# Kernel optimization log

Hardware: AMD Instinct MI355X
Metric: run time of the kernel (lower is better)

## Reference

```python
import jax, jax.numpy as jnp
import numpy as np

E, C, H, I = 8, 4096, 1024, 4096

def setup_inputs() -> dict:
    key = jax.random.key(0)
    k_x, k_g, k_u, k_d = jax.random.split(key, 4)
    scale_h = 1.0 / np.sqrt(H)
    scale_i = 1.0 / np.sqrt(I)
    return {
        "x_routed": jax.random.normal(k_x, (E, C, H), dtype=jnp.float32),
        "W_gate": jax.random.normal(k_g, (E, H, I), dtype=jnp.float32) * scale_h,
        "W_up": jax.random.normal(k_u, (E, H, I), dtype=jnp.float32) * scale_h,
        "W_down": jax.random.normal(k_d, (E, I, H), dtype=jnp.float32) * scale_i,
    }

def reference(x_routed, W_gate, W_up, W_down):
    # Per-expert SwiGLU MLP, batched over the expert axis as a grouped GEMM.
    # gate = silu(x @ Wg); up = x @ Wu; out = (gate * up) @ Wd
    gate = jax.nn.silu(jnp.einsum("ech,ehi->eci", x_routed, W_gate))
    up = jnp.einsum("ech,ehi->eci", x_routed, W_up)
    out = jnp.einsum("eci,eih->ech", gate * up, W_down)
    return out
```

## Files before the change

kernel.cpp:

```cpp
#include <hip/hip_runtime.h>
#include <hip/hip_bf16.h>
#include <stdint.h>
#include <stddef.h>

#define E_ 8
#define C_ 4096
#define H_ 1024
#define I_ 4096

typedef short s16;
typedef __attribute__((ext_vector_type(8))) short short8;
typedef __attribute__((ext_vector_type(4))) short short4v;
typedef __attribute__((ext_vector_type(4))) float f32x4;
typedef __attribute__((ext_vector_type(4))) float float4v;

__device__ __forceinline__ s16 f2bf(float f) {
  union { __hip_bfloat16 h; s16 s; } u;
  u.h = __float2bfloat16(f);
  return u.s;
}

__device__ __forceinline__ void gload16(const void* gsrc, void* ldst) {
  __builtin_amdgcn_global_load_lds(
      (const __attribute__((address_space(1))) void*)gsrc,
      (__attribute__((address_space(3))) void*)ldst, 16, 0, 0);
}

__global__ __launch_bounds__(256) void prep_kernel(
    const float* __restrict__ x, const float* __restrict__ Wg,
    const float* __restrict__ Wu, const float* __restrict__ Wd,
    s16* __restrict__ xb, s16* __restrict__ Wgu, s16* __restrict__ WdT)
{
  __shared__ float tile[64][65];
  const int t = threadIdx.x;
  const int z = blockIdx.z;
  const size_t e = blockIdx.y;

  if (z == 0) {
    size_t base = e * (size_t)C_ * H_ + ((size_t)blockIdx.x * 256 + t) * 16;
    for (int j = 0; j < 16; j += 8) {
      float4v v0 = *(const float4v*)(x + base + j);
      float4v v1 = *(const float4v*)(x + base + j + 4);
      s16 o[8];
      o[0] = f2bf(v0[0]); o[1] = f2bf(v0[1]); o[2] = f2bf(v0[2]); o[3] = f2bf(v0[3]);
      o[4] = f2bf(v1[0]); o[5] = f2bf(v1[1]); o[6] = f2bf(v1[2]); o[7] = f2bf(v1[3]);
      *(short8*)(xb + base + j) = *(short8*)o;
    }
    return;
  }

  const float* src; int Cc;
  if (z == 1)      { src = Wg + e * (size_t)H_ * I_; Cc = I_; }
  else if (z == 2) { src = Wu + e * (size_t)H_ * I_; Cc = I_; }
  else             { src = Wd + e * (size_t)H_ * I_; Cc = H_; }

  const int tpr  = Cc >> 6;
  const int trow = blockIdx.x / tpr;
  const int tcol = blockIdx.x % tpr;

  const int c = t & 63, rq = t >> 6;
  for (int i = 0; i < 16; ++i) {
    int r = rq * 16 + i;
    tile[r][c] = src[(size_t)(trow * 64 + r) * Cc + tcol * 64 + c];
  }
  __syncthreads();

  const int ro = t >> 2, cb = (t & 3) * 16;
  s16 o[16];
  for (int j = 0; j < 16; ++j) o[j] = f2bf(tile[cb + j][ro]);

  const int i0 = tcol * 64 + ro;
  s16* op;
  if (z == 3) {
    op = WdT + e * (size_t)H_ * I_ + (size_t)i0 * I_ + trow * 64 + cb;
  } else {
    int grow = ((i0 & ~15) << 1) + (i0 & 15) + ((z == 2) ? 16 : 0);
    op = Wgu + e * (size_t)2 * I_ * H_ + (size_t)grow * H_ + trow * 64 + cb;
  }
  *(short8*)op       = *(short8*)&o[0];
  *(short8*)(op + 8) = *(short8*)&o[8];
}

#define MFMA16(MH, A0, A1, A2, A3)                                                            \
  acc[(MH)*4+0][0] = __builtin_amdgcn_mfma_f32_16x16x32_bf16(bf[0], A0, acc[(MH)*4+0][0],0,0,0); \
  acc[(MH)*4+0][1] = __builtin_amdgcn_mfma_f32_16x16x32_bf16(bf[1], A0, acc[(MH)*4+0][1],0,0,0); \
  acc[(MH)*4+0][2] = __builtin_amdgcn_mfma_f32_16x16x32_bf16(bf[2], A0, acc[(MH)*4+0][2],0,0,0); \
  acc[(MH)*4+0][3] = __builtin_amdgcn_mfma_f32_16x16x32_bf16(bf[3], A0, acc[(MH)*4+0][3],0,0,0); \
  acc[(MH)*4+1][0] = __builtin_amdgcn_mfma_f32_16x16x32_bf16(bf[0], A1, acc[(MH)*4+1][0],0,0,0); \
  acc[(MH)*4+1][1] = __builtin_amdgcn_mfma_f32_16x16x32_bf16(bf[1], A1, acc[(MH)*4+1][1],0,0,0); \
  acc[(MH)*4+1][2] = __builtin_amdgcn_mfma_f32_16x16x32_bf16(bf[2], A1, acc[(MH)*4+1][2],0,0,0); \
  acc[(MH)*4+1][3] = __builtin_amdgcn_mfma_f32_16x16x32_bf16(bf[3], A1, acc[(MH)*4+1][3],0,0,0); \
  acc[(MH)*4+2][0] = __builtin_amdgcn_mfma_f32_16x16x32_bf16(bf[0], A2, acc[(MH)*4+2][0],0,0,0); \
  acc[(MH)*4+2][1] = __builtin_amdgcn_mfma_f32_16x16x32_bf16(bf[1], A2, acc[(MH)*4+2][1],0,0,0); \
  acc[(MH)*4+2][2] = __builtin_amdgcn_mfma_f32_16x16x32_bf16(bf[2], A2, acc[(MH)*4+2][2],0,0,0); \
  acc[(MH)*4+2][3] = __builtin_amdgcn_mfma_f32_16x16x32_bf16(bf[3], A2, acc[(MH)*4+2][3],0,0,0); \
  acc[(MH)*4+3][0] = __builtin_amdgcn_mfma_f32_16x16x32_bf16(bf[0], A3, acc[(MH)*4+3][0],0,0,0); \
  acc[(MH)*4+3][1] = __builtin_amdgcn_mfma_f32_16x16x32_bf16(bf[1], A3, acc[(MH)*4+3][1],0,0,0); \
  acc[(MH)*4+3][2] = __builtin_amdgcn_mfma_f32_16x16x32_bf16(bf[2], A3, acc[(MH)*4+3][2],0,0,0); \
  acc[(MH)*4+3][3] = __builtin_amdgcn_mfma_f32_16x16x32_bf16(bf[3], A3, acc[(MH)*4+3][3],0,0,0);

#define VMW4 asm volatile("s_waitcnt vmcnt(4)" ::: "memory");
#define VMW6 asm volatile("s_waitcnt vmcnt(6)" ::: "memory");

#define LDA32(B, MH, M) \
  (*(const short8*)(shm + (B)*8192 + aBase + (MH)*2048 + (M)*512))
#define LDB32(B, N) \
  (*(const short8*)(shm + 16384 + (B)*4096 + bBase + (N)*512))

__global__ __launch_bounds__(256, 2) void gemm_gu(
    const s16* __restrict__ Abase, const s16* __restrict__ Bbase,
    s16* __restrict__ HOut)
{
  constexpr int K   = H_;
  constexpr int NB  = 2 * I_;
  constexpr int NT  = K / 32;

  __shared__ s16 shm[24576];

  const int tid  = threadIdx.x;
  const int wave = tid >> 6, lane = tid & 63;
  const int e    = blockIdx.z;

  const int bid = blockIdx.x;
  const int xcd = bid & 7;
  const int idx = bid >> 3;
  const int bn  = xcd * 8 + (idx & 7);
  const int bm  = idx >> 3;

  const s16* A = Abase + (size_t)e * C_ * K + (size_t)bm * 256 * K;
  const s16* B = Bbase + (size_t)e * NB * K + (size_t)bn * 128 * K;

  const int wm = (wave >> 1) * 128;
  const int wn = (wave & 1) * 64;
  const int lr  = lane & 15;
  const int lkb = (lane >> 4) * 8;

  const int qA    = (((lr & 1) << 5) | lkb) ^ ((lr >> 1) << 3);
  const int aBase = (wm << 5) + ((lr >> 1) << 6) + qA;
  const int bBase = (wn << 5) + ((lr >> 1) << 6) + qA;

  const int l     = lane;
  const int inner = (((l & 7) ^ (l >> 3)) << 3);
  const int rloc  = ((l >> 3) << 1) | (inner >> 5);
  const int ck    = inner & 31;
  const int sdst  = wave * 512;

  auto stageA = [&](int kt, int b) {
    #pragma unroll
    for (int ch = 0; ch < 4; ++ch)
      gload16(A + (size_t)(ch * 64 + wave * 16 + rloc) * K + kt * 32 + ck,
              shm + b * 8192 + ch * 2048 + sdst);
  };
  auto stageB = [&](int kt, int b) {
    #pragma unroll
    for (int ch = 0; ch < 2; ++ch)
      gload16(B + (size_t)(ch * 64 + wave * 16 + rloc) * K + kt * 32 + ck,
              shm + 16384 + b * 4096 + ch * 2048 + sdst);
  };

  f32x4 acc[8][4];
  #pragma unroll
  for (int m = 0; m < 8; ++m)
    #pragma unroll
    for (int n = 0; n < 4; ++n) acc[m][n] = (f32x4){0.f, 0.f, 0.f, 0.f};

  stageA(0, 0);
  stageB(0, 0);

  short8 bf[4];
  for (int t = 0; t < NT; ++t) {
    const int b  = t & 1;
    const int tn = (t + 1 < NT) ? (t + 1) : (NT - 1);
    stageA(tn, b ^ 1);
    stageB(tn, b ^ 1);
    VMW6
    __builtin_amdgcn_sched_barrier(0);
    __builtin_amdgcn_s_barrier();
    bf[0] = LDB32(b, 0); bf[1] = LDB32(b, 1);
    bf[2] = LDB32(b, 2); bf[3] = LDB32(b, 3);
    {
      short8 a0 = LDA32(b, 0, 0), a1 = LDA32(b, 0, 1);
      short8 a2 = LDA32(b, 0, 2), a3 = LDA32(b, 0, 3);
      asm volatile("s_waitcnt lgkmcnt(0)" ::: "memory");
      __builtin_amdgcn_sched_barrier(0);
      __builtin_amdgcn_s_setprio(1);
      MFMA16(0, a0, a1, a2, a3)
    }
    {
      short8 a0 = LDA32(b, 1, 0), a1 = LDA32(b, 1, 1);
      short8 a2 = LDA32(b, 1, 2), a3 = LDA32(b, 1, 3);
      asm volatile("s_waitcnt lgkmcnt(0)" ::: "memory");
      __builtin_amdgcn_sched_barrier(0);
      MFMA16(1, a0, a1, a2, a3)
      __builtin_amdgcn_s_setprio(0);
    }
    __builtin_amdgcn_sched_barrier(0);
    __builtin_amdgcn_s_barrier();
  }

  const int lcc = (lane >> 4) * 4;
  s16* Hp = HOut + (size_t)e * C_ * I_;
  const int ibase = bn * 64 + (wn >> 1);
  #pragma unroll
  for (int m = 0; m < 8; ++m) {
    const int row = bm * 256 + wm + m * 16 + lr;
    #pragma unroll
    for (int p = 0; p < 2; ++p) {
      const int col = ibase + p * 16 + lcc;
      s16 o4[4];
      #pragma unroll
      for (int q = 0; q < 4; ++q) {
        float g = acc[m][2 * p][q], u = acc[m][2 * p + 1][q];
        float sg = 1.0f / (1.0f + __expf(-g));
        o4[q] = f2bf(g * sg * u);
      }
      __builtin_nontemporal_store(*(short4v*)o4,
                                  (short4v*)(Hp + (size_t)row * I_ + col));
    }
  }
}

#define LDAF(B, MH, M, CX) \
  (*(const short8*)(shm + (B)*16384 + ((wm + (MH)*64 + (M)*16 + lr) << 6) + (CX)))
#define LDBF(B, N, CX) \
  (*(const short8*)(shm + 32768 + (B)*16384 + ((wn + (N)*16 + lr) << 6) + (CX)))

#define PHASE(B, MH, CX, RDB, STMT, WV)                                      \
  {                                                                          \
    short8 af0 = LDAF(B, MH, 0, CX);                                         \
    short8 af1 = LDAF(B, MH, 1, CX);                                         \
    short8 af2 = LDAF(B, MH, 2, CX);                                         \
    short8 af3 = LDAF(B, MH, 3, CX);                                         \
    if (RDB) {                                                               \
      bf[0] = LDBF(B, 0, CX); bf[1] = LDBF(B, 1, CX);                        \
      bf[2] = LDBF(B, 2, CX); bf[3] = LDBF(B, 3, CX);                        \
    }                                                                        \
    STMT                                                                     \
    __builtin_amdgcn_sched_barrier(0);                                       \
    __builtin_amdgcn_s_barrier();                                            \
    asm volatile("s_waitcnt lgkmcnt(0)" ::: "memory");                       \
    __builtin_amdgcn_sched_barrier(0);                                       \
    __builtin_amdgcn_s_setprio(1);                                           \
    MFMA16(MH, af0, af1, af2, af3)                                           \
    __builtin_amdgcn_s_setprio(0);                                           \
    __builtin_amdgcn_sched_barrier(0);                                       \
    WV                                                                       \
    __builtin_amdgcn_s_barrier();                                            \
  }

__global__ __launch_bounds__(512, 2) void gemm_dn(
    const s16* __restrict__ Abase, const s16* __restrict__ Bbase,
    float* __restrict__ FOut)
{
  constexpr int K  = I_;
  constexpr int NB = H_;
  constexpr int NT = K / 64;
  constexpr int TN = NB / 256;
  constexpr int TM = C_ / 256;
  constexpr int NWG = TM * TN;

  __shared__ s16 shm[65536];

  const int tid  = threadIdx.x;
  const int wave = tid >> 6, lane = tid & 63;
  const int e    = blockIdx.z;

  const int bid = blockIdx.x;
  const int swz = (bid & 7) * (NWG / 8) + (bid >> 3);
  const int bm = swz / TN, bn = swz % TN;

  const s16* A = Abase + (size_t)e * C_ * K + (size_t)bm * 256 * K;
  const s16* B = Bbase + (size_t)e * NB * K + (size_t)bn * 256 * K;

  const int wm  = (wave >> 2) * 128;
  const int wn  = (wave & 3) * 64;
  const int lr  = lane & 15;
  const int lkb = (lane >> 4) * 8;
  const int xr  = (lr & 7) << 3;
  const int cx0 = lkb ^ xr;
  const int cx1 = (32 + lkb) ^ xr;

  const int srow = tid >> 3;
  const int scol = ((tid & 7) ^ (srow & 7)) * 8;
  const size_t stoff = (size_t)srow * K + scol;
  const int sdst = wave * 512;

  auto stageA = [&](int kt, int b) {
    #pragma unroll
    for (int h = 0; h < 2; ++h)
      #pragma unroll
      for (int ll = 0; ll < 2; ++ll)
        gload16(A + (size_t)(h * 128 + ll * 64) * K + (size_t)kt * 64 + stoff,
                shm + b * 16384 + h * 8192 + ll * 4096 + sdst);
  };
  auto stageB = [&](int kt, int b) {
    #pragma unroll
    for (int h = 0; h < 2; ++h)
      #pragma unroll
      for (int ll = 0; ll < 2; ++ll)
        gload16(B + (size_t)(h * 128 + ll * 64) * K + (size_t)kt * 64 + stoff,
                shm + 32768 + b * 16384 + h * 8192 + ll * 4096 + sdst);
  };

  f32x4 acc[8][4];
  #pragma unroll
  for (int m = 0; m < 8; ++m)
    #pragma unroll
    for (int n = 0; n < 4; ++n) acc[m][n] = (f32x4){0.f, 0.f, 0.f, 0.f};

  stageB(0, 0);
  stageA(0, 0);
  stageB(1, 1);
  VMW4
  __builtin_amdgcn_sched_barrier(0);
  __builtin_amdgcn_s_barrier();

  short8 bf[4];
  for (int i = 0; i < NT / 2; ++i) {
    const int t1 = 2 * i + 1;
    const int t2 = (2 * i + 2 < NT) ? (2 * i + 2) : (NT - 1);
    const int t3 = (2 * i + 3 < NT) ? (2 * i + 3) : (NT - 1);
    PHASE(0, 0, cx0, 1, { stageA(t1, 1); }, )
    PHASE(0, 1, cx0, 0, {}, )
    PHASE(0, 0, cx1, 1, {}, )
    PHASE(0, 1, cx1, 0, { stageB(t2, 0); }, VMW4)
    PHASE(1, 0, cx0, 1, { stageA(t2, 0); }, )
    PHASE(1, 1, cx0, 0, {}, )
    PHASE(1, 0, cx1, 1, {}, )
    PHASE(1, 1, cx1, 0, { stageB(t3, 1); }, VMW4)
  }

  const int lcc = (lane >> 4) * 4;
  float* Op = FOut + (size_t)e * C_ * H_;
  #pragma unroll
  for (int m = 0; m < 8; ++m) {
    const int row = bm * 256 + wm + m * 16 + lr;
    #pragma unroll
    for (int n = 0; n < 4; ++n) {
      const int col = bn * 256 + wn + n * 16 + lcc;
      __builtin_nontemporal_store(acc[m][n],
                                  (float4v*)(Op + (size_t)row * H_ + col));
    }
  }
}

extern "C" void kernel_launch(void* const* d_in, const int* in_sizes, int n_in,
                              void* d_out, int out_size, void* d_ws, size_t ws_size,
                              hipStream_t stream) {
  const float* x  = (const float*)d_in[0];
  const float* Wg = (const float*)d_in[1];
  const float* Wu = (const float*)d_in[2];
  const float* Wd = (const float*)d_in[3];
  float* out = (float*)d_out;

  const size_t szX  = (size_t)C_ * H_;
  const size_t szGU = (size_t)2 * I_ * H_;
  const size_t szWd = (size_t)H_ * I_;
  const size_t szH  = (size_t)C_ * I_;

  const size_t needFull = 2 * E_ * (szX + szGU + szWd + szH);

  constexpr int GU_BLK = (C_ / 256) * ((2 * I_) / 128);
  constexpr int DN_BLK = (C_ / 256) * (H_ / 256);

  if (ws_size >= needFull) {
    s16* xb  = (s16*)d_ws;
    s16* Wgu = xb  + E_ * szX;
    s16* WdT = Wgu + E_ * szGU;
    s16* hbf = WdT + E_ * szWd;

    prep_kernel<<<dim3(1024, E_, 4), 256, 0, stream>>>(
        x, Wg, Wu, Wd, xb, Wgu, WdT);
    gemm_gu<<<dim3(GU_BLK, 1, E_), 256, 0, stream>>>(
        xb, Wgu, hbf);
    gemm_dn<<<dim3(DN_BLK, 1, E_), 512, 0, stream>>>(
        hbf, WdT, out);
  } else {
    s16* xb  = (s16*)d_ws;
    s16* Wgu = xb  + szX;
    s16* WdT = Wgu + szGU;
    s16* hbf = WdT + szWd;

    for (int e = 0; e < E_; ++e) {
      prep_kernel<<<dim3(1024, 1, 4), 256, 0, stream>>>(
          x + e * szX, Wg + e * szWd, Wu + e * szWd, Wd + e * szWd,
          xb, Wgu, WdT);
      gemm_gu<<<dim3(GU_BLK, 1, 1), 256, 0, stream>>>(
          xb, Wgu, hbf);
      gemm_dn<<<dim3(DN_BLK, 1, 1), 512, 0, stream>>>(
          hbf, WdT, out + e * szX);
    }
  }
}
```

Measured before the change: 1.023 ms.

## Enlarge gate/up GEMM tile to 256x256 with 8 waves and 4-stage LDS pipeline

The gate/up GEMM block grows from 256x128 with 4 waves to 256x256 with 8 waves, which halves the number of blocks and raises reuse of each A and B tile. The double-buffered LDS staging becomes a 4-deep ring (128 KB of shared memory) with three tiles prefetched, one barrier per K step, and all fragment loads issued before the MFMAs. The block-to-XCD mapping is changed so each XCD covers a 2D patch of tiles, and nontemporal stores are replaced with plain stores in both GEMMs. The risks are lower occupancy from the large LDS footprint and two resident blocks per CU possibly not fitting, plus fewer blocks to spread across CUs.

```diff
diff --git a/kernel.cpp b/kernel.cpp
--- a/kernel.cpp
+++ b/kernel.cpp
@@ -100,22 +100,22 @@
   acc[(MH)*4+3][3] = __builtin_amdgcn_mfma_f32_16x16x32_bf16(bf[3], A3, acc[(MH)*4+3][3],0,0,0);
 
 #define VMW4 asm volatile("s_waitcnt vmcnt(4)" ::: "memory");
-#define VMW6 asm volatile("s_waitcnt vmcnt(6)" ::: "memory");
-
-#define LDA32(B, MH, M) \
-  (*(const short8*)(shm + (B)*8192 + aBase + (MH)*2048 + (M)*512))
-#define LDB32(B, N) \
-  (*(const short8*)(shm + 16384 + (B)*4096 + bBase + (N)*512))
-
-__global__ __launch_bounds__(256, 2) void gemm_gu(
+#define VMW8 asm volatile("s_waitcnt vmcnt(8)" ::: "memory");
+
+#define LDA32(BUF, MH, M) \
+  (*(const short8*)(shm + (BUF)*8192 + aBase + (MH)*2048 + (M)*512))
+#define LDB32(BUF, N) \
+  (*(const short8*)(shm + 32768 + (BUF)*8192 + bBase + (N)*512))
+
+__global__ __launch_bounds__(512, 2) void gemm_gu(
     const s16* __restrict__ Abase, const s16* __restrict__ Bbase,
     s16* __restrict__ HOut)
 {
-  constexpr int K   = H_;
-  constexpr int NB  = 2 * I_;
-  constexpr int NT  = K / 32;
-
-  __shared__ s16 shm[24576];
+  constexpr int K  = H_;
+  constexpr int NB = 2 * I_;
+  constexpr int NT = K / 32;
+
+  __shared__ s16 shm[65536];
 
   const int tid  = threadIdx.x;
   const int wave = tid >> 6, lane = tid & 63;
@@ -124,14 +124,14 @@
   const int bid = blockIdx.x;
   const int xcd = bid & 7;
   const int idx = bid >> 3;
-  const int bn  = xcd * 8 + (idx & 7);
-  const int bm  = idx >> 3;
+  const int bn  = (xcd & 3) * 8 + (idx & 7);
+  const int bm  = (xcd >> 2) * 8 + (idx >> 3);
 
   const s16* A = Abase + (size_t)e * C_ * K + (size_t)bm * 256 * K;
-  const s16* B = Bbase + (size_t)e * NB * K + (size_t)bn * 128 * K;
-
-  const int wm = (wave >> 1) * 128;
-  const int wn = (wave & 1) * 64;
+  const s16* B = Bbase + (size_t)e * NB * K + (size_t)bn * 256 * K;
+
+  const int wm  = (wave >> 2) * 128;
+  const int wn  = (wave & 3) * 64;
   const int lr  = lane & 15;
   const int lkb = (lane >> 4) * 8;
 
@@ -139,23 +139,19 @@
   const int aBase = (wm << 5) + ((lr >> 1) << 6) + qA;
   const int bBase = (wn << 5) + ((lr >> 1) << 6) + qA;
 
-  const int l     = lane;
-  const int inner = (((l & 7) ^ (l >> 3)) << 3);
-  const int rloc  = ((l >> 3) << 1) | (inner >> 5);
-  const int ck    = inner & 31;
-  const int sdst  = wave * 512;
-
-  auto stageA = [&](int kt, int b) {
-    #pragma unroll
-    for (int ch = 0; ch < 4; ++ch)
-      gload16(A + (size_t)(ch * 64 + wave * 16 + rloc) * K + kt * 32 + ck,
-              shm + b * 8192 + ch * 2048 + sdst);
-  };
-  auto stageB = [&](int kt, int b) {
-    #pragma unroll
-    for (int ch = 0; ch < 2; ++ch)
-      gload16(B + (size_t)(ch * 64 + wave * 16 + rloc) * K + kt * 32 + ck,
-              shm + 16384 + b * 4096 + ch * 2048 + sdst);
+  const int u    = (lane & 7) ^ (lane >> 3);
+  const int srcR = 2 * (lane >> 3) + (u >> 2);
+  const int srcK = (u & 3) * 8;
+  const int sdst = wave * 512;
+
+  auto stage = [&](int kt, int b) {
+    #pragma unroll
+    for (int ch = 0; ch < 2; ++ch) {
+      const size_t roff = (size_t)(ch * 128 + wave * 16 + srcR) * K
+                        + (size_t)kt * 32 + srcK;
+      gload16(A + roff, shm + b * 8192 + ch * 4096 + sdst);
+      gload16(B + roff, shm + 32768 + b * 8192 + ch * 4096 + sdst);
+    }
   };
 
   f32x4 acc[8][4];
@@ -164,43 +160,38 @@
     #pragma unroll
     for (int n = 0; n < 4; ++n) acc[m][n] = (f32x4){0.f, 0.f, 0.f, 0.f};
 
-  stageA(0, 0);
-  stageB(0, 0);
+  stage(0, 0);
+  stage(1, 1);
+  stage(2, 2);
+  VMW8
+  __builtin_amdgcn_sched_barrier(0);
+  __builtin_amdgcn_s_barrier();
 
   short8 bf[4];
   for (int t = 0; t < NT; ++t) {
-    const int b  = t & 1;
-    const int tn = (t + 1 < NT) ? (t + 1) : (NT - 1);
-    stageA(tn, b ^ 1);
-    stageB(tn, b ^ 1);
-    VMW6
-    __builtin_amdgcn_sched_barrier(0);
-    __builtin_amdgcn_s_barrier();
+    const int b  = t & 3;
+    const int tp = (t + 3 < NT) ? (t + 3) : (NT - 1);
+    short8 a00 = LDA32(b, 0, 0), a01 = LDA32(b, 0, 1);
+    short8 a02 = LDA32(b, 0, 2), a03 = LDA32(b, 0, 3);
+    short8 a10 = LDA32(b, 1, 0), a11 = LDA32(b, 1, 1);
+    short8 a12 = LDA32(b, 1, 2), a13 = LDA32(b, 1, 3);
     bf[0] = LDB32(b, 0); bf[1] = LDB32(b, 1);
     bf[2] = LDB32(b, 2); bf[3] = LDB32(b, 3);
-    {
-      short8 a0 = LDA32(b, 0, 0), a1 = LDA32(b, 0, 1);
-      short8 a2 = LDA32(b, 0, 2), a3 = LDA32(b, 0, 3);
-      asm volatile("s_waitcnt lgkmcnt(0)" ::: "memory");
-      __builtin_amdgcn_sched_barrier(0);
-      __builtin_amdgcn_s_setprio(1);
-      MFMA16(0, a0, a1, a2, a3)
-    }
-    {
-      short8 a0 = LDA32(b, 1, 0), a1 = LDA32(b, 1, 1);
-      short8 a2 = LDA32(b, 1, 2), a3 = LDA32(b, 1, 3);
-      asm volatile("s_waitcnt lgkmcnt(0)" ::: "memory");
-      __builtin_amdgcn_sched_barrier(0);
-      MFMA16(1, a0, a1, a2, a3)
-      __builtin_amdgcn_s_setprio(0);
-    }
+    stage(tp, (t + 3) & 3);
+    asm volatile("s_waitcnt lgkmcnt(0)" ::: "memory");
     __builtin_amdgcn_sched_barrier(0);
+    __builtin_amdgcn_s_setprio(1);
+    MFMA16(0, a00, a01, a02, a03)
+    MFMA16(1, a10, a11, a12, a13)
+    __builtin_amdgcn_s_setprio(0);
+    __builtin_amdgcn_sched_barrier(0);
+    VMW8
     __builtin_amdgcn_s_barrier();
   }
 
   const int lcc = (lane >> 4) * 4;
   s16* Hp = HOut + (size_t)e * C_ * I_;
-  const int ibase = bn * 64 + (wn >> 1);
+  const int ibase = bn * 128 + (wn >> 1);
   #pragma unroll
   for (int m = 0; m < 8; ++m) {
     const int row = bm * 256 + wm + m * 16 + lr;
@@ -210,12 +201,11 @@
       s16 o4[4];
       #pragma unroll
       for (int q = 0; q < 4; ++q) {
-        float g = acc[m][2 * p][q], u = acc[m][2 * p + 1][q];
+        float g = acc[m][2 * p][q], uv = acc[m][2 * p + 1][q];
         float sg = 1.0f / (1.0f + __expf(-g));
-        o4[q] = f2bf(g * sg * u);
+        o4[q] = f2bf(g * sg * uv);
       }
-      __builtin_nontemporal_store(*(short4v*)o4,
-                                  (short4v*)(Hp + (size_t)row * I_ + col));
+      *(short4v*)(Hp + (size_t)row * I_ + col) = *(short4v*)o4;
     }
   }
 }
@@ -338,8 +328,7 @@
     #pragma unroll
     for (int n = 0; n < 4; ++n) {
       const int col = bn * 256 + wn + n * 16 + lcc;
-      __builtin_nontemporal_store(acc[m][n],
-                                  (float4v*)(Op + (size_t)row * H_ + col));
+      *(float4v*)(Op + (size_t)row * H_ + col) = acc[m][n];
     }
   }
 }
@@ -360,7 +349,7 @@
 
   const size_t needFull = 2 * E_ * (szX + szGU + szWd + szH);
 
-  constexpr int GU_BLK = (C_ / 256) * ((2 * I_) / 128);
+  constexpr int GU_BLK = (C_ / 256) * (2 * I_ / 256);
   constexpr int DN_BLK = (C_ / 256) * (H_ / 256);
 
   if (ws_size >= needFull) {
@@ -371,7 +360,7 @@
 
     prep_kernel<<<dim3(1024, E_, 4), 256, 0, stream>>>(
         x, Wg, Wu, Wd, xb, Wgu, WdT);
-    gemm_gu<<<dim3(GU_BLK, 1, E_), 256, 0, stream>>>(
+    gemm_gu<<<dim3(GU_BLK, 1, E_), 512, 0, stream>>>(
         xb, Wgu, hbf);
     gemm_dn<<<dim3(DN_BLK, 1, E_), 512, 0, stream>>>(
         hbf, WdT, out);
@@ -385,7 +374,7 @@
       prep_kernel<<<dim3(1024, 1, 4), 256, 0, stream>>>(
           x + e * szX, Wg + e * szWd, Wu + e * szWd, Wd + e * szWd,
           xb, Wgu, WdT);
-      gemm_gu<<<dim3(GU_BLK, 1, 1), 256, 0, stream>>>(
+      gemm_gu<<<dim3(GU_BLK, 1, 1), 512, 0, stream>>>(
           xb, Wgu, hbf);
       gemm_dn<<<dim3(DN_BLK, 1, 1), 512, 0, stream>>>(
           hbf, WdT, out + e * szX);
```

After: 990.5 us. 3.2% less time.
